# Kernel tuning notes

Hardware: AMD Instinct MI355X
Metric: run time of the kernel (lower is better)

## Reference

```python
import jax, jax.numpy as jnp
import numpy as np

N_NODES = 50000


def gcn_conv(x, row, col, ew, W, b):
    # PyG GCNConv with edge_weight: add self-loops (weight 1), symmetric norm,
    # then scatter-add of normalized messages at target nodes.
    n = x.shape[0]
    loop = jnp.arange(n)
    row_f = jnp.concatenate([row, loop])
    col_f = jnp.concatenate([col, loop])
    w_f = jnp.concatenate([ew, jnp.ones((n,), dtype=x.dtype)])
    deg = jax.ops.segment_sum(w_f, col_f, num_segments=n)  # [N]
    dinv = jnp.where(deg > 0, jax.lax.rsqrt(deg), jnp.zeros_like(deg))
    norm = dinv[row_f] * w_f * dinv[col_f]                 # [E+N]
    h = x @ W                                              # [N, out]
    msgs = h[row_f] * norm[:, None]                        # gather + weight
    out = jax.ops.segment_sum(msgs, col_f, num_segments=n) # scatter_add
    return out + b


def setup_inputs() -> dict:
    key = jax.random.key(0)
    ks = jax.random.split(key, 12)
    E = 1600000
    nf, ef, efil, nfil, classes = 128, 16, 32, 128, 40
    x = jax.random.normal(ks[0], (N_NODES, nf), dtype=jnp.float32)
    edge_index = jax.random.randint(ks[1], (2, E), 0, N_NODES, dtype=jnp.int64)
    edge_x = jax.random.normal(ks[2], (E, ef), dtype=jnp.float32)
    def lin(k, fan_in, shape):
        bound = 1.0 / np.sqrt(fan_in)
        return jax.random.uniform(k, shape, jnp.float32, -bound, bound)
    W1 = lin(ks[3], ef, (ef, efil)); b1 = lin(ks[4], ef, (efil,))
    W2 = lin(ks[5], efil, (efil, 1)); b2 = lin(ks[6], efil, (1,))
    Wg1 = lin(ks[7], nf, (nf, nfil)); bg1 = jnp.zeros((nfil,), jnp.float32)
    Wg2 = lin(ks[8], nfil, (nfil, classes)); bg2 = jnp.zeros((classes,), jnp.float32)
    return {"x": x, "edge_index": edge_index, "edge_x": edge_x,
            "W1": W1, "b1": b1, "W2": W2, "b2": b2,
            "Wg1": Wg1, "bg1": bg1, "Wg2": Wg2, "bg2": bg2}


def reference(x, edge_index, edge_x, W1, b1, W2, b2, Wg1, bg1, Wg2, bg2):
    row, col = edge_index[0], edge_index[1]
    # edge-weight MLP: relu -> sigmoid scalar per edge
    e = jax.nn.relu(edge_x @ W1 + b1)
    ew = jax.nn.sigmoid(e @ W2 + b2).reshape(-1)  # [E]
    h = gcn_conv(x, row, col, ew, Wg1, bg1)
    h = jax.nn.relu(h)
    # F.dropout(training=self.training): identity at inference
    out = gcn_conv(h, row, col, ew, Wg2, bg2)
    return out
```

## Files before the change

kernel.cpp:

```cpp
#include <hip/hip_runtime.h>
#include <hip/hip_bf16.h>
#include <math.h>


#define NF   128
#define EF   16
#define EFIL 32
#define NCLS 40
#define TILE 4096

__device__ inline unsigned pack_bf16x2(float a, float b) {
    unsigned ua = __float_as_uint(a);
    unsigned ub = __float_as_uint(b);
    ua += 0x7FFF + ((ua >> 16) & 1);
    ub += 0x7FFF + ((ub >> 16) & 1);
    return (ua >> 16) | (ub & 0xFFFF0000u);
}
__device__ inline float bf16_lo(unsigned u) { return __uint_as_float(u << 16); }
__device__ inline float bf16_hi(unsigned u) { return __uint_as_float(u & 0xFFFF0000u); }

__global__ __launch_bounds__(256) void edge_mlp_kernel(
    const float* __restrict__ ex, const float* __restrict__ W1,
    const float* __restrict__ b1, const float* __restrict__ W2,
    const float* __restrict__ b2, float* __restrict__ ew, int E)
{
    __shared__ float sW1[EF * EFIL];
    __shared__ float sb1[EFIL];
    __shared__ float sW2[EFIL];
    __shared__ float sb2;
    int t = threadIdx.x;
    for (int i = t; i < EF * EFIL; i += 256) sW1[i] = W1[i];
    if (t < EFIL) { sb1[t] = b1[t]; sW2[t] = W2[t]; }
    if (t == 0) sb2 = b2[0];
    __syncthreads();

    int e = blockIdx.x * 256 + t;
    if (e >= E) return;

    float xv[EF];
    const float4* exv = (const float4*)(ex) + (size_t)e * (EF / 4);
    #pragma unroll
    for (int q = 0; q < EF / 4; q++) {
        float4 v = exv[q];
        xv[q * 4 + 0] = v.x; xv[q * 4 + 1] = v.y;
        xv[q * 4 + 2] = v.z; xv[q * 4 + 3] = v.w;
    }
    float acc = sb2;
    #pragma unroll
    for (int j = 0; j < EFIL; j++) {
        float h = sb1[j];
        #pragma unroll
        for (int k = 0; k < EF; k++) h += xv[k] * sW1[k * EFIL + j];
        acc += fmaxf(h, 0.0f) * sW2[j];
    }
    ew[e] = 1.0f / (1.0f + expf(-acc));
}

__global__ __launch_bounds__(256) void hist1_kernel(
    const int* __restrict__ col, int* __restrict__ hist, int E, int ntiles)
{
    __shared__ int h[256];
    int t = threadIdx.x;
    h[t] = 0;
    __syncthreads();
    int tile = blockIdx.x;
    int base = tile * TILE;
    int end = base + TILE; if (end > E) end = E;
    for (int i = base + t; i < end; i += 256)
        atomicAdd(&h[col[i] >> 8], 1);
    __syncthreads();
    hist[t * ntiles + tile] = h[t];
}

__global__ __launch_bounds__(256) void scanA_kernel(
    int* __restrict__ hist, int* __restrict__ dtot, int ntiles)
{
    __shared__ int ts[256];
    int d = blockIdx.x;
    int t = threadIdx.x;
    int* hrow = hist + (size_t)d * ntiles;
    int C = (ntiles + 255) >> 8;
    int b = t * C;
    int e = b + C; if (e > ntiles) e = ntiles;
    int s = 0;
    for (int i = b; i < e; i++) s += hrow[i];
    ts[t] = s;
    __syncthreads();
    for (int dd = 1; dd < 256; dd <<= 1) {
        int v = (t >= dd) ? ts[t - dd] : 0;
        __syncthreads();
        ts[t] += v;
        __syncthreads();
    }
    int run = ts[t] - s;
    for (int i = b; i < e; i++) {
        int v = hrow[i];
        hrow[i] = run;
        run += v;
    }
    if (t == 255) dtot[d] = ts[255];
}

__global__ __launch_bounds__(256) void scanB_kernel(
    const int* __restrict__ dtot, int* __restrict__ dbase, int E)
{
    __shared__ int ts[256];
    int t = threadIdx.x;
    int s = dtot[t];
    ts[t] = s;
    __syncthreads();
    for (int dd = 1; dd < 256; dd <<= 1) {
        int v = (t >= dd) ? ts[t - dd] : 0;
        __syncthreads();
        ts[t] += v;
        __syncthreads();
    }
    dbase[t] = ts[t] - s;
    if (t == 255) dbase[256] = E;
}

__global__ __launch_bounds__(256) void scatter1_kernel(
    const int* __restrict__ row, const int* __restrict__ col,
    const float* __restrict__ ew, const int* __restrict__ hscan,
    const int* __restrict__ dbase,
    int* __restrict__ keyS, int* __restrict__ srcS, float* __restrict__ ewS,
    int E, int ntiles)
{
    __shared__ int cur[256];
    int t = threadIdx.x;
    int tile = blockIdx.x;
    cur[t] = dbase[t] + hscan[t * ntiles + tile];
    __syncthreads();
    int base = tile * TILE;
    int end = base + TILE; if (end > E) end = E;
    for (int i = base + t; i < end; i += 256) {
        int c = col[i];
        int p = atomicAdd(&cur[c >> 8], 1);
        keyS[p] = c;
        srcS[p] = row[i];
        ewS[p] = ew[i];
    }
}

__global__ __launch_bounds__(512) void bucket_sort_kernel(
    const int* __restrict__ keyS, const int* __restrict__ srcS,
    const float* __restrict__ ewS, const int* __restrict__ dbase,
    int* __restrict__ srcF, float* __restrict__ wgtF,
    int* __restrict__ offs, float* __restrict__ dinv,
    int E, int N)
{
    __shared__ int   cnt[256];
    __shared__ int   scan[256];
    __shared__ int   cursor[256];
    __shared__ float dsum[256];
    __shared__ float sdinv[256];
    int t = threadIdx.x;
    int b = blockIdx.x;
    if (t == 0 && b == 0) offs[N] = E;
    int bstart = dbase[b];
    int bend   = dbase[b + 1];
    if (t < 256) { cnt[t] = 0; dsum[t] = 0.0f; sdinv[t] = 0.0f; }
    __syncthreads();
    for (int i = bstart + t; i < bend; i += 512) {
        int lo = keyS[i] & 255;
        atomicAdd(&cnt[lo], 1);
        atomicAdd(&dsum[lo], ewS[i]);
    }
    __syncthreads();
    if (t < 256) scan[t] = cnt[t];
    __syncthreads();
    for (int d = 1; d < 256; d <<= 1) {
        int v = 0;
        if (t < 256 && t >= d) v = scan[t - d];
        __syncthreads();
        if (t < 256) scan[t] += v;
        __syncthreads();
    }
    if (t < 256) {
        int excl = scan[t] - cnt[t];
        int c = (b << 8) + t;
        cursor[t] = bstart + excl;
        if (c < N) {
            offs[c] = bstart + excl;
            float deg = 1.0f + dsum[t];
            float di = rsqrtf(deg);
            sdinv[t] = di;
            dinv[c] = di;
        }
    }
    __syncthreads();
    for (int i = bstart + t; i < bend; i += 512) {
        int k = keyS[i];
        int lo = k & 255;
        int p = atomicAdd(&cursor[lo], 1);
        srcF[p] = srcS[i];
        wgtF[p] = ewS[i] * sdinv[lo];
    }
}

#define G1_ROWS 64
#define XPAD 68
__global__ __launch_bounds__(256, 4) void gemm1_kernel(
    const float* __restrict__ x, const float* __restrict__ W,
    const float* __restrict__ dinv, unsigned short* __restrict__ h1b, int N)
{
    __shared__ float sx[NF * XPAD];
    int t = threadIdx.x;
    int row0 = blockIdx.x * G1_ROWS;
    for (int i = t; i < G1_ROWS * NF; i += 256) {
        int r = i >> 7, k = i & 127;
        int gr = row0 + r;
        sx[k * XPAD + r] = (gr < N) ? x[(size_t)gr * NF + k] : 0.0f;
    }
    __syncthreads();

    int fg = t & 31, rg = t >> 5;
    int f0 = fg * 4, r0 = rg * 8;
    float acc[8][4];
    #pragma unroll
    for (int r = 0; r < 8; r++)
        #pragma unroll
        for (int c = 0; c < 4; c++) acc[r][c] = 0.0f;

    #pragma unroll 8
    for (int k = 0; k < NF; k++) {
        float4 w  = *(const float4*)&W[(size_t)k * NF + f0];
        float4 xa = *(const float4*)&sx[k * XPAD + r0];
        float4 xb = *(const float4*)&sx[k * XPAD + r0 + 4];
        float xr[8] = {xa.x, xa.y, xa.z, xa.w, xb.x, xb.y, xb.z, xb.w};
        #pragma unroll
        for (int r = 0; r < 8; r++) {
            acc[r][0] += xr[r] * w.x;
            acc[r][1] += xr[r] * w.y;
            acc[r][2] += xr[r] * w.z;
            acc[r][3] += xr[r] * w.w;
        }
    }
    #pragma unroll
    for (int r = 0; r < 8; r++) {
        int gr = row0 + r0 + r;
        if (gr < N) {
            float di = dinv[gr];
            uint2 p;
            p.x = pack_bf16x2(acc[r][0] * di, acc[r][1] * di);
            p.y = pack_bf16x2(acc[r][2] * di, acc[r][3] * di);
            *(uint2*)(h1b + (size_t)gr * NF + f0) = p;
        }
    }
}

__global__ __launch_bounds__(256) void gather1_kernel(
    const int* __restrict__ offs, const int* __restrict__ src,
    const float* __restrict__ wgt, const unsigned short* __restrict__ h1b,
    const float* __restrict__ dinv, const float* __restrict__ bg1,
    float* __restrict__ out1, int N)
{
    int wid  = threadIdx.x >> 6;
    int lane = threadIdx.x & 63;
    int c = blockIdx.x * 4 + wid;
    if (c >= N) return;
    float di = dinv[c];
    unsigned hu = *(const unsigned*)(h1b + (size_t)c * NF + 2 * lane);
    float2 acc;
    acc.x = bg1[2 * lane]     + bf16_lo(hu) * di;
    acc.y = bg1[2 * lane + 1] + bf16_hi(hu) * di;

    int beg = offs[c], end = offs[c + 1];
    for (int e0 = beg; e0 < end; e0 += 64) {
        int idx = e0 + lane;
        int   sv = 0; float wv = 0.0f;
        if (idx < end) { sv = src[idx]; wv = wgt[idx]; }
        int m = end - e0; if (m > 64) m = 64;
        int j = 0;
        for (; j + 8 <= m; j += 8) {
            unsigned v[8]; float w[8];
            #pragma unroll
            for (int u = 0; u < 8; u++) {
                int s = __shfl(sv, j + u);
                w[u] = __shfl(wv, j + u);
                v[u] = *(const unsigned*)(h1b + (size_t)s * NF + 2 * lane);
            }
            #pragma unroll
            for (int u = 0; u < 8; u++) {
                acc.x += w[u] * bf16_lo(v[u]);
                acc.y += w[u] * bf16_hi(v[u]);
            }
        }
        for (; j < m; j++) {
            int   s = __shfl(sv, j);
            float w = __shfl(wv, j);
            unsigned v = *(const unsigned*)(h1b + (size_t)s * NF + 2 * lane);
            acc.x += w * bf16_lo(v);
            acc.y += w * bf16_hi(v);
        }
    }
    *(float2*)(out1 + (size_t)c * NF + 2 * lane) = acc;
}

#define G2_ROWS 64
__global__ __launch_bounds__(256, 4) void gemm2_kernel(
    const float* __restrict__ out1, const float* __restrict__ W,
    const float* __restrict__ dinv, unsigned short* __restrict__ h2b, int N)
{
    __shared__ float sx[NF * XPAD];
    int t = threadIdx.x;
    int row0 = blockIdx.x * G2_ROWS;
    for (int i = t; i < G2_ROWS * NF; i += 256) {
        int r = i >> 7, k = i & 127;
        int gr = row0 + r;
        sx[k * XPAD + r] = (gr < N) ? fmaxf(out1[(size_t)gr * NF + k], 0.0f) : 0.0f;
    }
    __syncthreads();

    int fg = t & 15, rg = t >> 4;
    int f0 = fg * 4;
    int f0c = (f0 <= NCLS - 4) ? f0 : (NCLS - 4);
    int r0 = rg * 4;
    float acc[4][4];
    #pragma unroll
    for (int r = 0; r < 4; r++)
        #pragma unroll
        for (int c = 0; c < 4; c++) acc[r][c] = 0.0f;

    #pragma unroll 8
    for (int k = 0; k < NF; k++) {
        float4 w  = *(const float4*)&W[(size_t)k * NCLS + f0c];
        float4 xa = *(const float4*)&sx[k * XPAD + r0];
        float xr[4] = {xa.x, xa.y, xa.z, xa.w};
        #pragma unroll
        for (int r = 0; r < 4; r++) {
            acc[r][0] += xr[r] * w.x;
            acc[r][1] += xr[r] * w.y;
            acc[r][2] += xr[r] * w.z;
            acc[r][3] += xr[r] * w.w;
        }
    }
    if (f0 <= NCLS - 4) {
        #pragma unroll
        for (int r = 0; r < 4; r++) {
            int gr = row0 + r0 + r;
            if (gr < N) {
                float di = dinv[gr];
                uint2 p;
                p.x = pack_bf16x2(acc[r][0] * di, acc[r][1] * di);
                p.y = pack_bf16x2(acc[r][2] * di, acc[r][3] * di);
                *(uint2*)(h2b + (size_t)gr * NCLS + f0) = p;
            }
        }
    }
}

__global__ __launch_bounds__(256) void gather2_kernel(
    const int* __restrict__ offs, const int* __restrict__ src,
    const float* __restrict__ wgt, const unsigned short* __restrict__ h2b,
    const float* __restrict__ dinv, const float* __restrict__ bg2,
    float* __restrict__ out, int N)
{
    int wid  = threadIdx.x >> 6;
    int lane = threadIdx.x & 63;
    int c = blockIdx.x * 4 + wid;
    if (c >= N) return;
    float di = dinv[c];
    float2 acc = {0.0f, 0.0f};
    if (lane < NCLS / 2) {
        unsigned hu = *(const unsigned*)(h2b + (size_t)c * NCLS + 2 * lane);
        acc.x = bg2[2 * lane]     + bf16_lo(hu) * di;
        acc.y = bg2[2 * lane + 1] + bf16_hi(hu) * di;
    }

    int beg = offs[c], end = offs[c + 1];
    for (int e0 = beg; e0 < end; e0 += 64) {
        int idx = e0 + lane;
        int   sv = 0; float wv = 0.0f;
        if (idx < end) { sv = src[idx]; wv = wgt[idx]; }
        int m = end - e0; if (m > 64) m = 64;
        int j = 0;
        for (; j + 8 <= m; j += 8) {
            unsigned v[8]; float w[8];
            #pragma unroll
            for (int u = 0; u < 8; u++) {
                int s = __shfl(sv, j + u);
                w[u] = __shfl(wv, j + u);
                v[u] = (lane < NCLS / 2)
                     ? *(const unsigned*)(h2b + (size_t)s * NCLS + 2 * lane) : 0u;
            }
            #pragma unroll
            for (int u = 0; u < 8; u++) {
                acc.x += w[u] * bf16_lo(v[u]);
                acc.y += w[u] * bf16_hi(v[u]);
            }
        }
        for (; j < m; j++) {
            int   s = __shfl(sv, j);
            float w = __shfl(wv, j);
            if (lane < NCLS / 2) {
                unsigned v = *(const unsigned*)(h2b + (size_t)s * NCLS + 2 * lane);
                acc.x += w * bf16_lo(v);
                acc.y += w * bf16_hi(v);
            }
        }
    }
    if (lane < NCLS / 2) *(float2*)(out + (size_t)c * NCLS + 2 * lane) = acc;
}

extern "C" void kernel_launch(void* const* d_in, const int* in_sizes, int n_in,
                              void* d_out, int out_size, void* d_ws, size_t ws_size,
                              hipStream_t stream)
{
    const float* x   = (const float*)d_in[0];
    const int*   ei  = (const int*)d_in[1];
    const float* exf = (const float*)d_in[2];
    const float* W1  = (const float*)d_in[3];
    const float* b1  = (const float*)d_in[4];
    const float* W2  = (const float*)d_in[5];
    const float* b2  = (const float*)d_in[6];
    const float* Wg1 = (const float*)d_in[7];
    const float* bg1 = (const float*)d_in[8];
    const float* Wg2 = (const float*)d_in[9];
    const float* bg2 = (const float*)d_in[10];
    float* out = (float*)d_out;

    int N = in_sizes[0] / NF;
    int E = in_sizes[2] / EF;
    const int* row = ei;
    const int* col = ei + E;
    int ntiles = (E + TILE - 1) / TILE;
    int L = 256 * ntiles;

    char* base = (char*)d_ws;
    size_t off = 0;
    auto alloc = [&](size_t words) -> void* {
        void* p = base + off * 4;
        off += (words + 3) & ~(size_t)3;
        return p;
    };
    size_t awords = (size_t)4 * E;
    size_t hwords = ((size_t)N * NF + 1) / 2;
    if (hwords > awords) awords = hwords;
    float* regA = (float*)alloc(awords);
    float* ew   = regA;
    int*   keyS = (int*)(regA + E);
    int*   srcS = (int*)(regA + 2 * (size_t)E);
    float* ewS  = regA + 3 * (size_t)E;
    unsigned short* h1b = (unsigned short*)regA;
    unsigned short* h2b = (unsigned short*)regA;
    int*   srcF = (int*)  alloc(E);
    float* wgtF = (float*)alloc(E);
    float* out1 = (float*)alloc((size_t)N * NF);
    float* dinv = (float*)alloc(N);
    int*   offs = (int*)  alloc(N + 1);
    int*   hist = (int*)  alloc(L);
    int*   dtot = (int*)  alloc(256);
    int*   dbase= (int*)  alloc(257);

    int nb;
    nb = (E + 255) / 256;
    edge_mlp_kernel<<<nb, 256, 0, stream>>>(exf, W1, b1, W2, b2, ew, E);

    hist1_kernel<<<ntiles, 256, 0, stream>>>(col, hist, E, ntiles);
    scanA_kernel<<<256, 256, 0, stream>>>(hist, dtot, ntiles);
    scanB_kernel<<<1, 256, 0, stream>>>(dtot, dbase, E);
    scatter1_kernel<<<ntiles, 256, 0, stream>>>(row, col, ew, hist, dbase,
                                                keyS, srcS, ewS, E, ntiles);
    bucket_sort_kernel<<<256, 512, 0, stream>>>(keyS, srcS, ewS, dbase,
                                                srcF, wgtF, offs, dinv, E, N);

    nb = (N + G1_ROWS - 1) / G1_ROWS;
    gemm1_kernel<<<nb, 256, 0, stream>>>(x, Wg1, dinv, h1b, N);

    nb = (N + 3) / 4;
    gather1_kernel<<<nb, 256, 0, stream>>>(offs, srcF, wgtF, h1b, dinv, bg1, out1, N);

    nb = (N + G2_ROWS - 1) / G2_ROWS;
    gemm2_kernel<<<nb, 256, 0, stream>>>(out1, Wg2, dinv, h2b, N);

    nb = (N + 3) / 4;
    gather2_kernel<<<nb, 256, 0, stream>>>(offs, srcF, wgtF, h2b, dinv, bg2, out, N);
}
```

Before: 475.8 us.

## Pack edge arrays into AoS structs for sort and gather stages

Measured after the change: 432.6 us. 9.1% less time.

```diff
diff --git a/kernel.cpp b/kernel.cpp
--- a/kernel.cpp
+++ b/kernel.cpp
@@ -119,34 +119,31 @@
     if (t == 255) dbase[256] = E;
 }
 
-__global__ __launch_bounds__(256) void scatter1_kernel(
+__global__ __launch_bounds__(512) void scatter1_kernel(
     const int* __restrict__ row, const int* __restrict__ col,
     const float* __restrict__ ew, const int* __restrict__ hscan,
     const int* __restrict__ dbase,
-    int* __restrict__ keyS, int* __restrict__ srcS, float* __restrict__ ewS,
-    int E, int ntiles)
+    uint4* __restrict__ st, int E, int ntiles)
 {
     __shared__ int cur[256];
     int t = threadIdx.x;
     int tile = blockIdx.x;
-    cur[t] = dbase[t] + hscan[t * ntiles + tile];
+    if (t < 256) cur[t] = dbase[t] + hscan[t * ntiles + tile];
     __syncthreads();
     int base = tile * TILE;
     int end = base + TILE; if (end > E) end = E;
-    for (int i = base + t; i < end; i += 256) {
+    for (int i = base + t; i < end; i += 512) {
         int c = col[i];
+        int r = row[i];
+        float w = ew[i];
         int p = atomicAdd(&cur[c >> 8], 1);
-        keyS[p] = c;
-        srcS[p] = row[i];
-        ewS[p] = ew[i];
+        st[p] = make_uint4((unsigned)c, (unsigned)r, __float_as_uint(w), 0u);
     }
 }
 
 __global__ __launch_bounds__(512) void bucket_sort_kernel(
-    const int* __restrict__ keyS, const int* __restrict__ srcS,
-    const float* __restrict__ ewS, const int* __restrict__ dbase,
-    int* __restrict__ srcF, float* __restrict__ wgtF,
-    int* __restrict__ offs, float* __restrict__ dinv,
+    const uint4* __restrict__ st, const int* __restrict__ dbase,
+    uint2* __restrict__ edgeF, int* __restrict__ offs, float* __restrict__ dinv,
     int E, int N)
 {
     __shared__ int   cnt[256];
@@ -162,9 +159,10 @@
     if (t < 256) { cnt[t] = 0; dsum[t] = 0.0f; sdinv[t] = 0.0f; }
     __syncthreads();
     for (int i = bstart + t; i < bend; i += 512) {
-        int lo = keyS[i] & 255;
+        uint4 v = st[i];
+        int lo = (int)(v.x & 255u);
         atomicAdd(&cnt[lo], 1);
-        atomicAdd(&dsum[lo], ewS[i]);
+        atomicAdd(&dsum[lo], __uint_as_float(v.z));
     }
     __syncthreads();
     if (t < 256) scan[t] = cnt[t];
@@ -190,11 +188,11 @@
     }
     __syncthreads();
     for (int i = bstart + t; i < bend; i += 512) {
-        int k = keyS[i];
-        int lo = k & 255;
+        uint4 v = st[i];
+        int lo = (int)(v.x & 255u);
         int p = atomicAdd(&cursor[lo], 1);
-        srcF[p] = srcS[i];
-        wgtF[p] = ewS[i] * sdinv[lo];
+        float w = __uint_as_float(v.z) * sdinv[lo];
+        edgeF[p] = make_uint2(v.y, __float_as_uint(w));
     }
 }
 
@@ -250,8 +248,8 @@
 }
 
 __global__ __launch_bounds__(256) void gather1_kernel(
-    const int* __restrict__ offs, const int* __restrict__ src,
-    const float* __restrict__ wgt, const unsigned short* __restrict__ h1b,
+    const int* __restrict__ offs, const uint2* __restrict__ edgeF,
+    const unsigned short* __restrict__ h1b,
     const float* __restrict__ dinv, const float* __restrict__ bg1,
     float* __restrict__ out1, int N)
 {
@@ -268,8 +266,9 @@
     int beg = offs[c], end = offs[c + 1];
     for (int e0 = beg; e0 < end; e0 += 64) {
         int idx = e0 + lane;
-        int   sv = 0; float wv = 0.0f;
-        if (idx < end) { sv = src[idx]; wv = wgt[idx]; }
+        uint2 eg = make_uint2(0u, 0u);
+        if (idx < end) eg = edgeF[idx];
+        int sv = (int)eg.x; float wv = __uint_as_float(eg.y);
         int m = end - e0; if (m > 64) m = 64;
         int j = 0;
         for (; j + 8 <= m; j += 8) {
@@ -351,8 +350,8 @@
 }
 
 __global__ __launch_bounds__(256) void gather2_kernel(
-    const int* __restrict__ offs, const int* __restrict__ src,
-    const float* __restrict__ wgt, const unsigned short* __restrict__ h2b,
+    const int* __restrict__ offs, const uint2* __restrict__ edgeF,
+    const unsigned short* __restrict__ h2b,
     const float* __restrict__ dinv, const float* __restrict__ bg2,
     float* __restrict__ out, int N)
 {
@@ -371,8 +370,9 @@
     int beg = offs[c], end = offs[c + 1];
     for (int e0 = beg; e0 < end; e0 += 64) {
         int idx = e0 + lane;
-        int   sv = 0; float wv = 0.0f;
-        if (idx < end) { sv = src[idx]; wv = wgt[idx]; }
+        uint2 eg = make_uint2(0u, 0u);
+        if (idx < end) eg = edgeF[idx];
+        int sv = (int)eg.x; float wv = __uint_as_float(eg.y);
         int m = end - e0; if (m > 64) m = 64;
         int j = 0;
         for (; j + 8 <= m; j += 8) {
@@ -434,18 +434,14 @@
         off += (words + 3) & ~(size_t)3;
         return p;
     };
-    size_t awords = (size_t)4 * E;
+    float* ew   = (float*)alloc(E);
+    size_t stwords = (size_t)4 * E;
     size_t hwords = ((size_t)N * NF + 1) / 2;
-    if (hwords > awords) awords = hwords;
-    float* regA = (float*)alloc(awords);
-    float* ew   = regA;
-    int*   keyS = (int*)(regA + E);
-    int*   srcS = (int*)(regA + 2 * (size_t)E);
-    float* ewS  = regA + 3 * (size_t)E;
-    unsigned short* h1b = (unsigned short*)regA;
-    unsigned short* h2b = (unsigned short*)regA;
-    int*   srcF = (int*)  alloc(E);
-    float* wgtF = (float*)alloc(E);
+    if (hwords > stwords) stwords = hwords;
+    uint4* st   = (uint4*)alloc(stwords);
+    unsigned short* h1b = (unsigned short*)st;
+    unsigned short* h2b = (unsigned short*)st;
+    uint2* edgeF = (uint2*)alloc((size_t)2 * E);
     float* out1 = (float*)alloc((size_t)N * NF);
     float* dinv = (float*)alloc(N);
     int*   offs = (int*)  alloc(N + 1);
@@ -460,20 +456,19 @@
     hist1_kernel<<<ntiles, 256, 0, stream>>>(col, hist, E, ntiles);
     scanA_kernel<<<256, 256, 0, stream>>>(hist, dtot, ntiles);
     scanB_kernel<<<1, 256, 0, stream>>>(dtot, dbase, E);
-    scatter1_kernel<<<ntiles, 256, 0, stream>>>(row, col, ew, hist, dbase,
-                                                keyS, srcS, ewS, E, ntiles);
-    bucket_sort_kernel<<<256, 512, 0, stream>>>(keyS, srcS, ewS, dbase,
-                                                srcF, wgtF, offs, dinv, E, N);
+    scatter1_kernel<<<ntiles, 512, 0, stream>>>(row, col, ew, hist, dbase,
+                                                st, E, ntiles);
+    bucket_sort_kernel<<<256, 512, 0, stream>>>(st, dbase, edgeF, offs, dinv, E, N);
 
     nb = (N + G1_ROWS - 1) / G1_ROWS;
     gemm1_kernel<<<nb, 256, 0, stream>>>(x, Wg1, dinv, h1b, N);
 
     nb = (N + 3) / 4;
-    gather1_kernel<<<nb, 256, 0, stream>>>(offs, srcF, wgtF, h1b, dinv, bg1, out1, N);
+    gather1_kernel<<<nb, 256, 0, stream>>>(offs, edgeF, h1b, dinv, bg1, out1, N);
 
     nb = (N + G2_ROWS - 1) / G2_ROWS;
     gemm2_kernel<<<nb, 256, 0, stream>>>(out1, Wg2, dinv, h2b, N);
 
     nb = (N + 3) / 4;
-    gather2_kernel<<<nb, 256, 0, stream>>>(offs, srcF, wgtF, h2b, dinv, bg2, out, N);
-}
+    gather2_kernel<<<nb, 256, 0, stream>>>(offs, edgeF, h2b, dinv, bg2, out, N);
+}
```
